# Kernel optimization log

Hardware: AMD Instinct MI355X
Metric: run time of the kernel (lower is better)

The kernel has to match this reference:

```python
import jax, jax.numpy as jnp
import numpy as np

EPS = 1e-10
N_USER, N_ITEM, D = 100000, 50000, 64
E_R, E_T = 500000, 250000


def setup_inputs() -> dict:
    key = jax.random.key(0)
    ks = jax.random.split(key, 32)
    f32 = jnp.float32
    inp = {
        'x_u': jax.random.normal(ks[0], (N_USER, D), f32),
        'x_i': jax.random.normal(ks[1], (N_ITEM, D), f32),
        'a_u': jax.random.normal(ks[2], (N_USER, D), f32),
        'a_i': jax.random.normal(ks[3], (N_ITEM, D), f32),
        't': jax.random.normal(ks[4], (N_USER, D), f32),
        'boun3': jax.random.uniform(ks[5], (E_R,), f32),
        'user_intent': 0.01 * jax.random.uniform(ks[6], (N_USER, D), f32),
        'item_intent': 0.01 * jax.random.uniform(ks[7], (N_ITEM, D), f32),
        'W_att_w': jax.random.normal(ks[8], (2 * D, 1), f32) * 0.05,
        'W_att_b': jax.random.normal(ks[9], (1,), f32) * 0.05,
        'W4_w': jax.random.normal(ks[10], (4 * D, 2 * D), f32) * 0.05,
        'W4_b': jax.random.normal(ks[11], (2 * D,), f32) * 0.05,
        'W5_w': jax.random.normal(ks[12], (2 * D, D), f32) * 0.05,
        'W5_b': jax.random.normal(ks[13], (D,), f32) * 0.05,
        'W6_w': jax.random.normal(ks[14], (D, 1), f32) * 0.05,
        'W6_b': jax.random.normal(ks[15], (1,), f32) * 0.05,
        'W_so_w': jax.random.normal(ks[16], (2 * D, D), f32) * 0.05,
        'W_so_b': jax.random.normal(ks[17], (D,), f32) * 0.05,
        'W_so2_w': jax.random.normal(ks[18], (D, 1), f32) * 0.05,
        'W_so2_b': jax.random.normal(ks[19], (1,), f32) * 0.05,
        'rated_src': jax.random.randint(ks[20], (E_R,), 0, N_USER, jnp.int32),
        'rated_dst': jax.random.randint(ks[21], (E_R,), 0, N_ITEM, jnp.int32),
        'tp_src': jax.random.randint(ks[22], (E_T,), 0, N_USER, jnp.int32),
        'tp_dst': jax.random.randint(ks[23], (E_T,), 0, N_USER, jnp.int32),
        'tn_src': jax.random.randint(ks[24], (E_T,), 0, N_USER, jnp.int32),
        'tn_dst': jax.random.randint(ks[25], (E_T,), 0, N_USER, jnp.int32),
    }
    return inp


def _trust_score(t, src, dst, W_so_w, W_so_b, W_so2_w, W_so2_b):
    # solinkpre: sigmoid(W_so2(W_so(cat(t_src, t_dst)))) per edge  -> [E]
    h = jnp.concatenate([t[src], t[dst]], axis=1)          # [E, 2D]
    h = h @ W_so_w + W_so_b                                # [E, D] (no activation, as in source)
    return jax.nn.sigmoid(h @ W_so2_w + W_so2_b)[:, 0]


def _rmse(label, pred):
    dis = label - pred + EPS
    return jnp.sqrt(jnp.sum(dis * dis) / pred.shape[0])


def reference(x_u, x_i, a_u, a_i, t, boun3, user_intent, item_intent,
              W_att_w, W_att_b, W4_w, W4_b, W5_w, W5_b, W6_w, W6_b,
              W_so_w, W_so_b, W_so2_w, W_so2_b,
              rated_src, rated_dst, tp_src, tp_dst, tn_src, tn_dst):
    n_item = x_i.shape[0]
    # simple_ls + fn.max reduce: per-edge rowwise dot (torch.diag(mm) -> vectorized),
    # segment-max onto dst item nodes
    sim_ls = jax.nn.sigmoid(jnp.sum(user_intent[rated_src] * x_i[rated_dst], axis=-1))  # [E_R]
    a_sim = jax.ops.segment_max(sim_ls, rated_dst, num_segments=n_item)                 # [n_item]
    # attitude: sigmoid(W_att(cat(a_src, a_dst)))
    att = jax.nn.sigmoid(
        jnp.concatenate([a_u[rated_src], a_i[rated_dst]], axis=1) @ W_att_w + W_att_b
    )[:, 0]                                                                             # [E_R]
    # linear_s: a_sim[dst] * where(att>=0.5, 0, -0)  (identically zero, kept faithful)
    score = a_sim[rated_dst] * jnp.where(att >= 0.5, 0.0, -0.0)
    # _add_influ_mlp_concat: W6(W5(W4(cat(item_intent[dst], x_src, x_dst, user_intent[src]))))
    h = jnp.concatenate(
        [item_intent[rated_dst], x_u[rated_src], x_i[rated_dst], user_intent[rated_src]], axis=1
    )                                                                                   # [E_R, 4D]
    influ = (((h @ W4_w + W4_b) @ W5_w + W5_b) @ W6_w + W6_b)[:, 0]
    pos_score = score + influ
    # attitude RMSE against boun3 labels
    l_att = _rmse(boun3, att)
    # trust link prediction on pos and neg graphs
    pos_t = _trust_score(t, tp_src, tp_dst, W_so_w, W_so_b, W_so2_w, W_so2_b)
    neg_t = _trust_score(t, tn_src, tn_dst, W_so_w, W_so_b, W_so2_w, W_so2_b)
    score_t = jnp.concatenate([pos_t, neg_t])
    label = jnp.concatenate([jnp.ones_like(pos_t), jnp.zeros_like(neg_t)])
    loss_trust = _rmse(label, score_t)
    # roc_auc / average_precision (jnp equivalents of sklearn metrics)
    n = score_t.shape[0]
    P = jnp.sum(label)
    N = n - P
    order = jnp.argsort(score_t)
    ranks = jnp.zeros(n, score_t.dtype).at[order].set(jnp.arange(1, n + 1, dtype=score_t.dtype))
    auc = (jnp.sum(ranks * label) - P * (P + 1) / 2) / (P * N)
    desc = jnp.argsort(-score_t)
    l_sorted = label[desc]
    prec = jnp.cumsum(l_sorted) / jnp.arange(1, n + 1, dtype=score_t.dtype)
    ap = jnp.sum(prec * l_sorted) / P
    return pos_score, l_att, auc, ap, loss_trust
```

## Files before the change

### kernel.cpp

```cpp
#include <hip/hip_runtime.h>

#define N_USER 100000
#define N_ITEM 50000
#define E_R    500000
#define E_T    250000
#define NB     (1 << 20)
#define NCH    4096
#define ZMIN   (-4.0f)
#define ZSCALE ((float)NB / 8.0f)
#define UW     12500
#define IW     6250
#define TW     (UW + IW)
#define NODE_BLOCKS ((TW + 3) / 4)

__device__ __forceinline__ float sigmoidf(float z) {
  return 1.0f / (1.0f + expf(-z));
}

__device__ __forceinline__ float dot4(float4 a, float4 b) {
  return a.x * b.x + a.y * b.y + a.z * b.z + a.w * b.w;
}

__device__ __forceinline__ float wave_sum_f(float v) {
#pragma unroll
  for (int off = 32; off > 0; off >>= 1) v += __shfl_xor(v, off, 64);
  return v;
}

__device__ __forceinline__ unsigned wave_sum_u(unsigned v) {
#pragma unroll
  for (int off = 32; off > 0; off >>= 1) v += __shfl_xor(v, off, 64);
  return v;
}

__device__ __forceinline__ double wave_sum_d(double v) {
#pragma unroll
  for (int off = 32; off > 0; off >>= 1) v += __shfl_xor(v, off, 64);
  return v;
}

__global__ void k_collapse(const float* __restrict__ W4w, const float* __restrict__ W4b,
                           const float* __restrict__ W5w, const float* __restrict__ W5b,
                           const float* __restrict__ W6w, const float* __restrict__ W6b,
                           const float* __restrict__ Wsow, const float* __restrict__ Wsob,
                           const float* __restrict__ Wso2w, const float* __restrict__ Wso2b,
                           float* __restrict__ wts) {
  __shared__ float v56[128];
  int t = threadIdx.x;
  if (t < 128) {
    float s = 0.f;
    for (int k = 0; k < 64; ++k) s += W5w[t * 64 + k] * W6w[k];
    v56[t] = s;
  }
  __syncthreads();
  {
    float s = 0.f;
    for (int j = 0; j < 128; ++j) s += W4w[t * 128 + j] * v56[j];
    wts[t] = s;
  }
  if (t < 128) {
    float s = 0.f;
    for (int k = 0; k < 64; ++k) s += Wsow[t * 64 + k] * Wso2w[k];
    wts[320 + t] = s;
  }
  if (t < 64) {
    float pb = W5b[t] * W6w[t] + W4b[t] * v56[t] + W4b[64 + t] * v56[64 + t];
    float ps = Wsob[t] * Wso2w[t];
    pb = wave_sum_f(pb);
    ps = wave_sum_f(ps);
    if (t == 0) {
      wts[256] = pb + W6b[0];
      wts[448] = ps + Wso2b[0];
    }
  }
}

__global__ void k_nodes(const float* __restrict__ xu, const float* __restrict__ ui,
                        const float* __restrict__ au, const float* __restrict__ tt,
                        const float* __restrict__ xi, const float* __restrict__ ii,
                        const float* __restrict__ ai,
                        const float* __restrict__ Wattw, const float* __restrict__ wts,
                        float2* __restrict__ u_rate, float2* __restrict__ u_trust,
                        float2* __restrict__ i_rate,
                        uint2* __restrict__ hz) {
  int idx = blockIdx.x * 256 + threadIdx.x;
  if (idx < NB) hz[idx] = make_uint2(0u, 0u);

  int lane = threadIdx.x & 63;
  int wave = blockIdx.x * 4 + (threadIdx.x >> 6);
  if (wave >= TW) return;
  int g = lane >> 4;
  int q = lane & 15;

  if (wave < UW) {
    const float4* xu4 = (const float4*)xu;
    const float4* ui4 = (const float4*)ui;
    const float4* au4 = (const float4*)au;
    const float4* tt4 = (const float4*)tt;
    int nA = wave * 8 + g;
    int baseA = nA * 16 + q;
    int baseB = baseA + 64;
    float4 xA = xu4[baseA], xB = xu4[baseB];
    float4 uA = ui4[baseA], uB = ui4[baseB];
    float4 aA = au4[baseA], aB = au4[baseB];
    float4 tA = tt4[baseA], tB = tt4[baseB];
    float4 wex = ((const float4*)(wts + 64))[q];
    float4 weu = ((const float4*)(wts + 192))[q];
    float4 wa  = ((const float4*)Wattw)[q];
    float4 w1  = ((const float4*)(wts + 320))[q];
    float4 w2  = ((const float4*)(wts + 384))[q];
    float sA0 = dot4(xA, wex) + dot4(uA, weu);
    float sB0 = dot4(xB, wex) + dot4(uB, weu);
    float sA1 = dot4(aA, wa), sB1 = dot4(aB, wa);
    float sA2 = dot4(tA, w1), sB2 = dot4(tB, w1);
    float sA3 = dot4(tA, w2), sB3 = dot4(tB, w2);
#pragma unroll
    for (int off = 1; off < 16; off <<= 1) {
      sA0 += __shfl_xor(sA0, off, 64); sB0 += __shfl_xor(sB0, off, 64);
      sA1 += __shfl_xor(sA1, off, 64); sB1 += __shfl_xor(sB1, off, 64);
      sA2 += __shfl_xor(sA2, off, 64); sB2 += __shfl_xor(sB2, off, 64);
      sA3 += __shfl_xor(sA3, off, 64); sB3 += __shfl_xor(sB3, off, 64);
    }
    if (q == 0) {
      u_rate[nA]      = make_float2(sA0, sA1);
      u_trust[nA]     = make_float2(sA2, sA3);
      u_rate[nA + 4]  = make_float2(sB0, sB1);
      u_trust[nA + 4] = make_float2(sB2, sB3);
    }
  } else {
    const float4* xi4 = (const float4*)xi;
    const float4* ii4 = (const float4*)ii;
    const float4* ai4 = (const float4*)ai;
    int nA = (wave - UW) * 8 + g;
    int baseA = nA * 16 + q;
    int baseB = baseA + 64;
    float4 xA = xi4[baseA], xB = xi4[baseB];
    float4 iA = ii4[baseA], iB = ii4[baseB];
    float4 aA = ai4[baseA], aB = ai4[baseB];
    float4 wei  = ((const float4*)(wts + 0))[q];
    float4 wexi = ((const float4*)(wts + 128))[q];
    float4 wai  = ((const float4*)(Wattw + 64))[q];
    float sA0 = dot4(iA, wei) + dot4(xA, wexi);
    float sB0 = dot4(iB, wei) + dot4(xB, wexi);
    float sA1 = dot4(aA, wai), sB1 = dot4(aB, wai);
#pragma unroll
    for (int off = 1; off < 16; off <<= 1) {
      sA0 += __shfl_xor(sA0, off, 64); sB0 += __shfl_xor(sB0, off, 64);
      sA1 += __shfl_xor(sA1, off, 64); sB1 += __shfl_xor(sB1, off, 64);
    }
    if (q == 0) {
      i_rate[nA]     = make_float2(sA0, sA1);
      i_rate[nA + 4] = make_float2(sB0, sB1);
    }
  }
}

__global__ void k_edges(const int* __restrict__ src, const int* __restrict__ dst,
                        const float* __restrict__ boun3,
                        const float2* __restrict__ u_rate, const float2* __restrict__ i_rate,
                        const int* __restrict__ tps, const int* __restrict__ tpd,
                        const int* __restrict__ tns, const int* __restrict__ tnd,
                        const float2* __restrict__ u_trust,
                        const float* __restrict__ wts, const float* __restrict__ Wattb,
                        float* __restrict__ out,
                        unsigned* __restrict__ histP, unsigned* __restrict__ histN,
                        double* __restrict__ partR, double* __restrict__ partT) {
  __shared__ double sd[4];
  float local = 0.f;
  if (blockIdx.x < 1024) {
    int e = blockIdx.x * 256 + threadIdx.x;
    if (e < E_R / 2) {
      float batt = Wattb[0];
      float beff = wts[256];
      int2 s = ((const int2*)src)[e], d = ((const int2*)dst)[e];
      float2 bo = ((const float2*)boun3)[e];
      float2 ur0 = u_rate[s.x], ur1 = u_rate[s.y];
      float2 ir0 = i_rate[d.x], ir1 = i_rate[d.y];
      ((float2*)out)[e] = make_float2(ur0.x + ir0.x + beff, ur1.x + ir1.x + beff);
      float d0 = bo.x - sigmoidf(ur0.y + ir0.y + batt) + 1e-10f;
      float d1 = bo.y - sigmoidf(ur1.y + ir1.y + batt) + 1e-10f;
      local = d0 * d0 + d1 * d1;
    }
    float w = wave_sum_f(local);
    if ((threadIdx.x & 63) == 0) sd[threadIdx.x >> 6] = (double)w;
    __syncthreads();
    if (threadIdx.x == 0) partR[blockIdx.x] = sd[0] + sd[1] + sd[2] + sd[3];
  } else {
    int b = blockIdx.x - 1024;
    int e = b * 256 + threadIdx.x;
    if (e < E_T) {
      float bso = wts[448];
      int2 s, d;
      int lab;
      if (e < E_T / 2) { s = ((const int2*)tps)[e]; d = ((const int2*)tpd)[e]; lab = 1; }
      else { s = ((const int2*)tns)[e - E_T / 2]; d = ((const int2*)tnd)[e - E_T / 2]; lab = 0; }
      unsigned* hist = lab ? histP : histN;
      float z0 = u_trust[s.x].x + u_trust[d.x].y + bso;
      float z1 = u_trust[s.y].x + u_trust[d.y].y + bso;
      float base = lab ? 1.0f : 0.0f;
      float d0 = base - sigmoidf(z0) + 1e-10f;
      float d1 = base - sigmoidf(z1) + 1e-10f;
      local = d0 * d0 + d1 * d1;
      int b0 = (int)((z0 - ZMIN) * ZSCALE); b0 = b0 < 0 ? 0 : (b0 >= NB ? NB - 1 : b0);
      int b1 = (int)((z1 - ZMIN) * ZSCALE); b1 = b1 < 0 ? 0 : (b1 >= NB ? NB - 1 : b1);
      atomicAdd(&hist[b0], 1u);
      atomicAdd(&hist[b1], 1u);
    }
    float w = wave_sum_f(local);
    if ((threadIdx.x & 63) == 0) sd[threadIdx.x >> 6] = (double)w;
    __syncthreads();
    if (threadIdx.x == 0) partT[b] = sd[0] + sd[1] + sd[2] + sd[3];
  }
}

__global__ void k_chunksum(const uint4* __restrict__ hP4, const uint4* __restrict__ hN4,
                           unsigned* __restrict__ chP, unsigned* __restrict__ chN) {
  int t = threadIdx.x, lane = t & 63, w = t >> 6;
  int chunk = blockIdx.x * 4 + w;
  int idx = chunk * 64 + lane;
  uint4 p = hP4[idx], n = hN4[idx];
  unsigned sp = p.x + p.y + p.z + p.w;
  unsigned sn = n.x + n.y + n.z + n.w;
  sp = wave_sum_u(sp);
  sn = wave_sum_u(sn);
  if (lane == 0) { chP[chunk] = sp; chN[chunk] = sn; }
}

__global__ void k_aucap(const unsigned* __restrict__ histP, const unsigned* __restrict__ histN,
                        const unsigned* __restrict__ chP, const unsigned* __restrict__ chN,
                        double* __restrict__ partC, double* __restrict__ partA) {
  int t = threadIdx.x, lane = t & 63, w = t >> 6;
  int blk = blockIdx.x;
  unsigned bp = 0, bn = 0;
  for (int c = t; c < blk; c += 256) { bp += chP[c]; bn += chN[c]; }
  bp = wave_sum_u(bp);
  bn = wave_sum_u(bn);
  __shared__ unsigned sbp[4], sbn[4], swp[4], swn[4];
  if (lane == 0) { sbp[w] = bp; sbn[w] = bn; }
  int bin = blk * 256 + t;
  unsigned np = histP[bin], nn = histN[bin];
  unsigned ip = np, in_ = nn;
#pragma unroll
  for (int off = 1; off < 64; off <<= 1) {
    int sl = lane >= off ? lane - off : lane;
    unsigned tp = __shfl(ip, sl, 64);
    unsigned tn = __shfl(in_, sl, 64);
    if (lane >= off) { ip += tp; in_ += tn; }
  }
  if (lane == 63) { swp[w] = ip; swn[w] = in_; }
  __syncthreads();
  unsigned base_p = sbp[0] + sbp[1] + sbp[2] + sbp[3];
  unsigned base_n = sbn[0] + sbn[1] + sbn[2] + sbn[3];
  unsigned wo_p = 0, wo_n = 0;
  for (int i = 0; i < 4; ++i) {
    if (i < w) { wo_p += swp[i]; wo_n += swn[i]; }
  }
  unsigned PA = base_p + wo_p + ip - np;
  unsigned NA = base_n + wo_n + in_ - nn;
  double Cc = (double)np * (double)NA + 0.5 * (double)np * (double)nn;
  double apc = 0.0;
  if (np > 0) {
    double cpa = (double)(E_T - PA - np);
    double cna = (double)(E_T - NA - nn);
    double ratio = (double)(np + nn) / (double)np;
    for (unsigned j = 1; j <= np; ++j) {
      double r = ((double)j - 0.5) * ratio + 0.5;
      apc += (cpa + (double)j) / (cpa + cna + r);
    }
  }
  double c = wave_sum_d(Cc);
  double a = wave_sum_d(apc);
  __shared__ double dc[4], da[4];
  if (lane == 0) { dc[w] = c; da[w] = a; }
  __syncthreads();
  if (t == 0) {
    partC[blk] = dc[0] + dc[1] + dc[2] + dc[3];
    partA[blk] = da[0] + da[1] + da[2] + da[3];
  }
}

__global__ void k_final(const double* __restrict__ partR, const double* __restrict__ partT,
                        const double* __restrict__ partC, const double* __restrict__ partA,
                        float* __restrict__ out) {
  int t = threadIdx.x;
  double sR = 0, sT = 0, sC = 0, sA = 0;
  for (int i = t; i < 1024; i += 256) { sR += partR[i]; sT += partT[i]; }
  for (int i = t; i < 4096; i += 256) { sC += partC[i]; sA += partA[i]; }
  sR = wave_sum_d(sR); sT = wave_sum_d(sT);
  sC = wave_sum_d(sC); sA = wave_sum_d(sA);
  __shared__ double sh[4][4];
  int lane = t & 63, w = t >> 6;
  if (lane == 0) { sh[w][0] = sR; sh[w][1] = sT; sh[w][2] = sC; sh[w][3] = sA; }
  __syncthreads();
  if (t == 0) {
    double R = sh[0][0] + sh[1][0] + sh[2][0] + sh[3][0];
    double T = sh[0][1] + sh[1][1] + sh[2][1] + sh[3][1];
    double C = sh[0][2] + sh[1][2] + sh[2][2] + sh[3][2];
    double A = sh[0][3] + sh[1][3] + sh[2][3] + sh[3][3];
    out[E_R + 0] = (float)sqrt(R / (double)E_R);
    out[E_R + 1] = (float)(C / ((double)E_T * (double)E_T));
    out[E_R + 2] = (float)(A / (double)E_T);
    out[E_R + 3] = (float)sqrt(T / (double)(2 * E_T));
  }
}

extern "C" void kernel_launch(void* const* d_in, const int* in_sizes, int n_in,
                              void* d_out, int out_size, void* d_ws, size_t ws_size,
                              hipStream_t stream) {
  (void)in_sizes; (void)n_in; (void)out_size; (void)ws_size;
  const float* x_u        = (const float*)d_in[0];
  const float* x_i        = (const float*)d_in[1];
  const float* a_u        = (const float*)d_in[2];
  const float* a_i        = (const float*)d_in[3];
  const float* t          = (const float*)d_in[4];
  const float* boun3      = (const float*)d_in[5];
  const float* user_int   = (const float*)d_in[6];
  const float* item_int   = (const float*)d_in[7];
  const float* W_att_w    = (const float*)d_in[8];
  const float* W_att_b    = (const float*)d_in[9];
  const float* W4_w       = (const float*)d_in[10];
  const float* W4_b       = (const float*)d_in[11];
  const float* W5_w       = (const float*)d_in[12];
  const float* W5_b       = (const float*)d_in[13];
  const float* W6_w       = (const float*)d_in[14];
  const float* W6_b       = (const float*)d_in[15];
  const float* W_so_w     = (const float*)d_in[16];
  const float* W_so_b     = (const float*)d_in[17];
  const float* W_so2_w    = (const float*)d_in[18];
  const float* W_so2_b    = (const float*)d_in[19];
  const int*   rated_src  = (const int*)d_in[20];
  const int*   rated_dst  = (const int*)d_in[21];
  const int*   tp_src     = (const int*)d_in[22];
  const int*   tp_dst     = (const int*)d_in[23];
  const int*   tn_src     = (const int*)d_in[24];
  const int*   tn_dst     = (const int*)d_in[25];
  float* out = (float*)d_out;

  char* ws = (char*)d_ws;
  double* partR   = (double*)ws;
  double* partT   = partR + 1024;
  double* partC   = partT + 1024;
  double* partA   = partC + 4096;
  unsigned* histP = (unsigned*)(partA + 4096);
  unsigned* histN = histP + NB;
  unsigned* chP   = histN + NB;
  unsigned* chN   = chP + NCH;
  float* wts      = (float*)(chN + NCH);
  float2* u_rate  = (float2*)(wts + 512);
  float2* u_trust = u_rate + N_USER;
  float2* i_rate  = u_trust + N_USER;

  k_collapse<<<1, 256, 0, stream>>>(W4_w, W4_b, W5_w, W5_b, W6_w, W6_b,
                                    W_so_w, W_so_b, W_so2_w, W_so2_b, wts);
  k_nodes<<<NODE_BLOCKS, 256, 0, stream>>>(x_u, user_int, a_u, t, x_i, item_int, a_i,
                                           W_att_w, wts, u_rate, u_trust, i_rate,
                                           (uint2*)histP);
  k_edges<<<2048, 256, 0, stream>>>(rated_src, rated_dst, boun3, u_rate, i_rate,
                                    tp_src, tp_dst, tn_src, tn_dst, u_trust,
                                    wts, W_att_b, out, histP, histN, partR, partT);
  k_chunksum<<<1024, 256, 0, stream>>>((const uint4*)histP, (const uint4*)histN, chP, chN);
  k_aucap<<<NCH, 256, 0, stream>>>(histP, histN, chP, chN, partC, partA);
  k_final<<<1, 256, 0, stream>>>(partR, partT, partC, partA, out);
}
```

Baseline: 264.6 us.

## Shrink AUC histogram, fuse chunk prefix into aucap, vectorize edge loads

The score histogram shrinks from 1M to 16K bins, so the zeroing pass and the AUC/AP scan touch far less memory. The separate chunk-sum kernel is removed: each aucap block now sums the whole small histogram itself to get its prefix base. Edge processing handles four edges per thread with int4/float4 loads, which halves the block count, and launch bounds are added. Coarser bins group more trust scores per bin, which may reduce how precisely AUC and AP match the reference.

```diff
diff --git a/kernel.cpp b/kernel.cpp
--- a/kernel.cpp
+++ b/kernel.cpp
@@ -4,14 +4,16 @@
 #define N_ITEM 50000
 #define E_R    500000
 #define E_T    250000
-#define NB     (1 << 20)
-#define NCH    4096
+#define NB     (1 << 14)
+#define NCH    64
 #define ZMIN   (-4.0f)
 #define ZSCALE ((float)NB / 8.0f)
 #define UW     12500
 #define IW     6250
 #define TW     (UW + IW)
 #define NODE_BLOCKS ((TW + 3) / 4)
+#define NBR    489
+#define NBT    489
 
 __device__ __forceinline__ float sigmoidf(float z) {
   return 1.0f / (1.0f + expf(-z));
@@ -75,16 +77,16 @@
   }
 }
 
-__global__ void k_nodes(const float* __restrict__ xu, const float* __restrict__ ui,
-                        const float* __restrict__ au, const float* __restrict__ tt,
-                        const float* __restrict__ xi, const float* __restrict__ ii,
-                        const float* __restrict__ ai,
-                        const float* __restrict__ Wattw, const float* __restrict__ wts,
-                        float2* __restrict__ u_rate, float2* __restrict__ u_trust,
-                        float2* __restrict__ i_rate,
-                        uint2* __restrict__ hz) {
-  int idx = blockIdx.x * 256 + threadIdx.x;
-  if (idx < NB) hz[idx] = make_uint2(0u, 0u);
+__global__ __launch_bounds__(256, 4)
+void k_nodes(const float* __restrict__ xu, const float* __restrict__ ui,
+             const float* __restrict__ au, const float* __restrict__ tt,
+             const float* __restrict__ xi, const float* __restrict__ ii,
+             const float* __restrict__ ai,
+             const float* __restrict__ Wattw, const float* __restrict__ wts,
+             float2* __restrict__ u_rate, float2* __restrict__ u_trust,
+             float2* __restrict__ i_rate,
+             uint4* __restrict__ hz) {
+  if (blockIdx.x < 32) hz[blockIdx.x * 256 + threadIdx.x] = make_uint4(0u, 0u, 0u, 0u);
 
   int lane = threadIdx.x & 63;
   int wave = blockIdx.x * 4 + (threadIdx.x >> 6);
@@ -155,56 +157,68 @@
   }
 }
 
-__global__ void k_edges(const int* __restrict__ src, const int* __restrict__ dst,
-                        const float* __restrict__ boun3,
-                        const float2* __restrict__ u_rate, const float2* __restrict__ i_rate,
-                        const int* __restrict__ tps, const int* __restrict__ tpd,
-                        const int* __restrict__ tns, const int* __restrict__ tnd,
-                        const float2* __restrict__ u_trust,
-                        const float* __restrict__ wts, const float* __restrict__ Wattb,
-                        float* __restrict__ out,
-                        unsigned* __restrict__ histP, unsigned* __restrict__ histN,
-                        double* __restrict__ partR, double* __restrict__ partT) {
+__global__ __launch_bounds__(256, 4)
+void k_edges(const int* __restrict__ src, const int* __restrict__ dst,
+             const float* __restrict__ boun3,
+             const float2* __restrict__ u_rate, const float2* __restrict__ i_rate,
+             const int* __restrict__ tps, const int* __restrict__ tpd,
+             const int* __restrict__ tns, const int* __restrict__ tnd,
+             const float2* __restrict__ u_trust,
+             const float* __restrict__ wts, const float* __restrict__ Wattb,
+             float* __restrict__ out,
+             unsigned* __restrict__ histP, unsigned* __restrict__ histN,
+             double* __restrict__ partR, double* __restrict__ partT) {
   __shared__ double sd[4];
   float local = 0.f;
-  if (blockIdx.x < 1024) {
+  if (blockIdx.x < NBR) {
     int e = blockIdx.x * 256 + threadIdx.x;
-    if (e < E_R / 2) {
+    if (e < E_R / 4) {
       float batt = Wattb[0];
       float beff = wts[256];
-      int2 s = ((const int2*)src)[e], d = ((const int2*)dst)[e];
-      float2 bo = ((const float2*)boun3)[e];
-      float2 ur0 = u_rate[s.x], ur1 = u_rate[s.y];
-      float2 ir0 = i_rate[d.x], ir1 = i_rate[d.y];
-      ((float2*)out)[e] = make_float2(ur0.x + ir0.x + beff, ur1.x + ir1.x + beff);
+      int4 s = ((const int4*)src)[e], d = ((const int4*)dst)[e];
+      float4 bo = ((const float4*)boun3)[e];
+      float2 ur0 = u_rate[s.x], ur1 = u_rate[s.y], ur2 = u_rate[s.z], ur3 = u_rate[s.w];
+      float2 ir0 = i_rate[d.x], ir1 = i_rate[d.y], ir2 = i_rate[d.z], ir3 = i_rate[d.w];
+      ((float4*)out)[e] = make_float4(ur0.x + ir0.x + beff, ur1.x + ir1.x + beff,
+                                      ur2.x + ir2.x + beff, ur3.x + ir3.x + beff);
       float d0 = bo.x - sigmoidf(ur0.y + ir0.y + batt) + 1e-10f;
       float d1 = bo.y - sigmoidf(ur1.y + ir1.y + batt) + 1e-10f;
-      local = d0 * d0 + d1 * d1;
+      float d2 = bo.z - sigmoidf(ur2.y + ir2.y + batt) + 1e-10f;
+      float d3 = bo.w - sigmoidf(ur3.y + ir3.y + batt) + 1e-10f;
+      local = d0 * d0 + d1 * d1 + d2 * d2 + d3 * d3;
     }
     float w = wave_sum_f(local);
     if ((threadIdx.x & 63) == 0) sd[threadIdx.x >> 6] = (double)w;
     __syncthreads();
     if (threadIdx.x == 0) partR[blockIdx.x] = sd[0] + sd[1] + sd[2] + sd[3];
   } else {
-    int b = blockIdx.x - 1024;
+    int b = blockIdx.x - NBR;
     int e = b * 256 + threadIdx.x;
-    if (e < E_T) {
+    if (e < 2 * E_T / 4) {
       float bso = wts[448];
-      int2 s, d;
+      int4 s, d;
       int lab;
-      if (e < E_T / 2) { s = ((const int2*)tps)[e]; d = ((const int2*)tpd)[e]; lab = 1; }
-      else { s = ((const int2*)tns)[e - E_T / 2]; d = ((const int2*)tnd)[e - E_T / 2]; lab = 0; }
+      if (e < E_T / 4) { s = ((const int4*)tps)[e]; d = ((const int4*)tpd)[e]; lab = 1; }
+      else { s = ((const int4*)tns)[e - E_T / 4]; d = ((const int4*)tnd)[e - E_T / 4]; lab = 0; }
       unsigned* hist = lab ? histP : histN;
       float z0 = u_trust[s.x].x + u_trust[d.x].y + bso;
       float z1 = u_trust[s.y].x + u_trust[d.y].y + bso;
+      float z2 = u_trust[s.z].x + u_trust[d.z].y + bso;
+      float z3 = u_trust[s.w].x + u_trust[d.w].y + bso;
       float base = lab ? 1.0f : 0.0f;
       float d0 = base - sigmoidf(z0) + 1e-10f;
       float d1 = base - sigmoidf(z1) + 1e-10f;
-      local = d0 * d0 + d1 * d1;
+      float d2 = base - sigmoidf(z2) + 1e-10f;
+      float d3 = base - sigmoidf(z3) + 1e-10f;
+      local = d0 * d0 + d1 * d1 + d2 * d2 + d3 * d3;
       int b0 = (int)((z0 - ZMIN) * ZSCALE); b0 = b0 < 0 ? 0 : (b0 >= NB ? NB - 1 : b0);
       int b1 = (int)((z1 - ZMIN) * ZSCALE); b1 = b1 < 0 ? 0 : (b1 >= NB ? NB - 1 : b1);
+      int b2 = (int)((z2 - ZMIN) * ZSCALE); b2 = b2 < 0 ? 0 : (b2 >= NB ? NB - 1 : b2);
+      int b3 = (int)((z3 - ZMIN) * ZSCALE); b3 = b3 < 0 ? 0 : (b3 >= NB ? NB - 1 : b3);
       atomicAdd(&hist[b0], 1u);
       atomicAdd(&hist[b1], 1u);
+      atomicAdd(&hist[b2], 1u);
+      atomicAdd(&hist[b3], 1u);
     }
     float w = wave_sum_f(local);
     if ((threadIdx.x & 63) == 0) sd[threadIdx.x >> 6] = (double)w;
@@ -213,30 +227,27 @@
   }
 }
 
-__global__ void k_chunksum(const uint4* __restrict__ hP4, const uint4* __restrict__ hN4,
-                           unsigned* __restrict__ chP, unsigned* __restrict__ chN) {
-  int t = threadIdx.x, lane = t & 63, w = t >> 6;
-  int chunk = blockIdx.x * 4 + w;
-  int idx = chunk * 64 + lane;
-  uint4 p = hP4[idx], n = hN4[idx];
-  unsigned sp = p.x + p.y + p.z + p.w;
-  unsigned sn = n.x + n.y + n.z + n.w;
-  sp = wave_sum_u(sp);
-  sn = wave_sum_u(sn);
-  if (lane == 0) { chP[chunk] = sp; chN[chunk] = sn; }
-}
-
-__global__ void k_aucap(const unsigned* __restrict__ histP, const unsigned* __restrict__ histN,
-                        const unsigned* __restrict__ chP, const unsigned* __restrict__ chN,
-                        double* __restrict__ partC, double* __restrict__ partA) {
+__global__ __launch_bounds__(256)
+void k_aucap(const uint4* __restrict__ hP4, const uint4* __restrict__ hN4,
+             const unsigned* __restrict__ histP, const unsigned* __restrict__ histN,
+             double* __restrict__ partC, double* __restrict__ partA) {
+  __shared__ unsigned qp[256], qn[256];
+  __shared__ unsigned sb[4][2], sw[4][2];
   int t = threadIdx.x, lane = t & 63, w = t >> 6;
   int blk = blockIdx.x;
-  unsigned bp = 0, bn = 0;
-  for (int c = t; c < blk; c += 256) { bp += chP[c]; bn += chN[c]; }
-  bp = wave_sum_u(bp);
-  bn = wave_sum_u(bn);
-  __shared__ unsigned sbp[4], sbn[4], swp[4], swn[4];
-  if (lane == 0) { sbp[w] = bp; sbn[w] = bn; }
+  unsigned sp = 0, sn = 0;
+#pragma unroll
+  for (int i = 0; i < 16; ++i) {
+    uint4 p = hP4[t * 16 + i], n = hN4[t * 16 + i];
+    sp += p.x + p.y + p.z + p.w;
+    sn += n.x + n.y + n.z + n.w;
+  }
+  qp[t] = sp; qn[t] = sn;
+  __syncthreads();
+  unsigned bp = (t < 4 * blk) ? qp[t] : 0u;
+  unsigned bn = (t < 4 * blk) ? qn[t] : 0u;
+  bp = wave_sum_u(bp); bn = wave_sum_u(bn);
+  if (lane == 0) { sb[w][0] = bp; sb[w][1] = bn; }
   int bin = blk * 256 + t;
   unsigned np = histP[bin], nn = histN[bin];
   unsigned ip = np, in_ = nn;
@@ -247,13 +258,13 @@
     unsigned tn = __shfl(in_, sl, 64);
     if (lane >= off) { ip += tp; in_ += tn; }
   }
-  if (lane == 63) { swp[w] = ip; swn[w] = in_; }
-  __syncthreads();
-  unsigned base_p = sbp[0] + sbp[1] + sbp[2] + sbp[3];
-  unsigned base_n = sbn[0] + sbn[1] + sbn[2] + sbn[3];
+  if (lane == 63) { sw[w][0] = ip; sw[w][1] = in_; }
+  __syncthreads();
+  unsigned base_p = sb[0][0] + sb[1][0] + sb[2][0] + sb[3][0];
+  unsigned base_n = sb[0][1] + sb[1][1] + sb[2][1] + sb[3][1];
   unsigned wo_p = 0, wo_n = 0;
   for (int i = 0; i < 4; ++i) {
-    if (i < w) { wo_p += swp[i]; wo_n += swn[i]; }
+    if (i < w) { wo_p += sw[i][0]; wo_n += sw[i][1]; }
   }
   unsigned PA = base_p + wo_p + ip - np;
   unsigned NA = base_n + wo_n + in_ - nn;
@@ -284,8 +295,9 @@
                         float* __restrict__ out) {
   int t = threadIdx.x;
   double sR = 0, sT = 0, sC = 0, sA = 0;
-  for (int i = t; i < 1024; i += 256) { sR += partR[i]; sT += partT[i]; }
-  for (int i = t; i < 4096; i += 256) { sC += partC[i]; sA += partA[i]; }
+  for (int i = t; i < NBR; i += 256) sR += partR[i];
+  for (int i = t; i < NBT; i += 256) sT += partT[i];
+  for (int i = t; i < NCH; i += 256) { sC += partC[i]; sA += partA[i]; }
   sR = wave_sum_d(sR); sT = wave_sum_d(sT);
   sC = wave_sum_d(sC); sA = wave_sum_d(sA);
   __shared__ double sh[4][4];
@@ -338,14 +350,12 @@
 
   char* ws = (char*)d_ws;
   double* partR   = (double*)ws;
-  double* partT   = partR + 1024;
-  double* partC   = partT + 1024;
-  double* partA   = partC + 4096;
-  unsigned* histP = (unsigned*)(partA + 4096);
+  double* partT   = partR + NBR;
+  double* partC   = partT + NBT;
+  double* partA   = partC + NCH;
+  unsigned* histP = (unsigned*)(partA + NCH);
   unsigned* histN = histP + NB;
-  unsigned* chP   = histN + NB;
-  unsigned* chN   = chP + NCH;
-  float* wts      = (float*)(chN + NCH);
+  float* wts      = (float*)(histN + NB);
   float2* u_rate  = (float2*)(wts + 512);
   float2* u_trust = u_rate + N_USER;
   float2* i_rate  = u_trust + N_USER;
@@ -354,11 +364,11 @@
                                     W_so_w, W_so_b, W_so2_w, W_so2_b, wts);
   k_nodes<<<NODE_BLOCKS, 256, 0, stream>>>(x_u, user_int, a_u, t, x_i, item_int, a_i,
                                            W_att_w, wts, u_rate, u_trust, i_rate,
-                                           (uint2*)histP);
-  k_edges<<<2048, 256, 0, stream>>>(rated_src, rated_dst, boun3, u_rate, i_rate,
-                                    tp_src, tp_dst, tn_src, tn_dst, u_trust,
-                                    wts, W_att_b, out, histP, histN, partR, partT);
-  k_chunksum<<<1024, 256, 0, stream>>>((const uint4*)histP, (const uint4*)histN, chP, chN);
-  k_aucap<<<NCH, 256, 0, stream>>>(histP, histN, chP, chN, partC, partA);
+                                           (uint4*)histP);
+  k_edges<<<NBR + NBT, 256, 0, stream>>>(rated_src, rated_dst, boun3, u_rate, i_rate,
+                                         tp_src, tp_dst, tn_src, tn_dst, u_trust,
+                                         wts, W_att_b, out, histP, histN, partR, partT);
+  k_aucap<<<NCH, 256, 0, stream>>>((const uint4*)histP, (const uint4*)histN,
+                                   histP, histN, partC, partA);
   k_final<<<1, 256, 0, stream>>>(partR, partT, partC, partA, out);
 }
```

Measured after the change: 344.5 us. +30.2%, slower.
